# Performance work log

Hardware: AMD Instinct MI355X
Metric: run time of the kernel (lower is better)

Reference implementation:

```python
import jax, jax.numpy as jnp
import numpy as np

# Dimensions (match init_kwargs / input_specs)
B, S, D = 4, 2048, 1024
H, DK = 16, 64
CL = 64            # chunk_len
C, N, NL = 32, 2, 128  # chunks, neighbors, neighbor_len
EPS = 1e-5
SCALE = 1.0 / np.sqrt(DK)


def setup_inputs() -> dict:
    key = jax.random.key(0)
    ks = jax.random.split(key, 8)
    w_in = 1.0 / np.sqrt(D)   # xavier-like scale for projections
    return {
        "h": jax.random.normal(ks[0], (B, S, D), jnp.float32),
        "e": jax.random.normal(ks[1], (B, C, N, NL, D), jnp.float32),
        "ln_g": jnp.ones((D,), jnp.float32),
        "ln_b": jnp.zeros((D,), jnp.float32),
        "Wq": jax.random.normal(ks[2], (D, H * DK), jnp.float32) * w_in,
        "bq": jnp.zeros((H * DK,), jnp.float32),
        "Wk": jax.random.normal(ks[3], (D, H * DK), jnp.float32) * w_in,
        "bk": jnp.zeros((H * DK,), jnp.float32),
        "Wv": jax.random.normal(ks[4], (D, H * DK), jnp.float32) * w_in,
        "bv": jnp.zeros((H * DK,), jnp.float32),
        "Wo": jax.random.normal(ks[5], (H * DK, D), jnp.float32) * (1.0 / np.sqrt(H * DK)),
        "bo": jnp.zeros((D,), jnp.float32),
    }


def _layernorm(x, g, b):
    mu = jnp.mean(x, axis=-1, keepdims=True)
    var = jnp.mean(jnp.square(x - mu), axis=-1, keepdims=True)
    return (x - mu) * jax.lax.rsqrt(var + EPS) * g + b


def reference(h, e, ln_g, ln_b, Wq, bq, Wk, bk, Wv, bv, Wo, bo):
    residual = h
    # shift queries so each chunk attends to neighbors retrieved for the previous chunk
    hs = _layernorm(h[:, CL - 1:], ln_g, ln_b)          # [B, S-CL+1, D]
    total = C * CL
    pad = max(0, total - hs.shape[1])
    hp = jnp.pad(hs, ((0, 0), (0, pad), (0, 0))) if pad > 0 else hs[:, :total]
    hb = hp.reshape(B, C, CL, D)                         # [B,C,CL,D]

    q = (hb @ Wq + bq).reshape(B, C, CL, H, DK)
    k = (e @ Wk + bk).reshape(B, C, N, NL, H, DK)
    v = (e @ Wv + bv).reshape(B, C, N, NL, H, DK)

    # scores: [B, C, H, CL, N, NL], softmax over merged (N, NL)
    attn = jnp.einsum('bcihd,bcnjhd->bchinj', q, k) * SCALE
    sh = attn.shape
    attn = jax.nn.softmax(attn.reshape(sh[0], sh[1], sh[2], sh[3], -1), axis=-1).reshape(sh)

    o = jnp.einsum('bchinj,bcnjhd->bcihd', attn, v).reshape(B, C * CL, H * DK)
    o = o @ Wo + bo                                      # [B, C*CL, D]
    # shift output back and crop to original length
    o = jnp.pad(o, ((0, 0), (CL - 1, 0), (0, 0)))[:, :S]
    return o + residual
```

## Files before the change

kernel.cpp:

```cpp
#include <hip/hip_runtime.h>


typedef __attribute__((ext_vector_type(8))) short short8;
typedef __attribute__((ext_vector_type(4))) float f32x4;
typedef unsigned short ushort_t;
typedef unsigned long long u64;

__device__ inline ushort_t f2bf(float f) {
  union { float f; unsigned int u; } v; v.f = f;
  unsigned int u = v.u;
  return (ushort_t)((u + 0x7fffu + ((u >> 16) & 1u)) >> 16);
}
__device__ inline float bf2f(ushort_t s) {
  union { unsigned int u; float f; } v; v.u = ((unsigned int)s) << 16;
  return v.f;
}

__device__ inline void gl_lds16(const void* g, void* l) {
  __builtin_amdgcn_global_load_lds(
      (const __attribute__((address_space(1))) unsigned int*)g,
      (__attribute__((address_space(3))) unsigned int*)l, 16, 0, 0);
}

__global__ void transpose_w4(const float* __restrict__ W0, const float* __restrict__ W1,
                             const float* __restrict__ W2, const float* __restrict__ W3,
                             ushort_t* __restrict__ T0, ushort_t* __restrict__ T1,
                             ushort_t* __restrict__ T2, ushort_t* __restrict__ T3) {
  __shared__ float tile[32][33];
  const int z = blockIdx.z;
  const float* W = (z == 0) ? W0 : (z == 1) ? W1 : (z == 2) ? W2 : W3;
  ushort_t* WT   = (z == 0) ? T0 : (z == 1) ? T1 : (z == 2) ? T2 : T3;
  int k0 = blockIdx.x * 32, n0 = blockIdx.y * 32;
  int c = threadIdx.x & 31, r = threadIdx.x >> 5;
#pragma unroll
  for (int p = 0; p < 4; p++)
    tile[r + p * 8][c] = W[(size_t)(k0 + r + p * 8) * 1024 + n0 + c];
  __syncthreads();
#pragma unroll
  for (int p = 0; p < 4; p++)
    WT[(size_t)(n0 + r + p * 8) * 1024 + k0 + c] = f2bf(tile[c][r + p * 8]);
}

__global__ void ln_kernel(const float* __restrict__ h, const float* __restrict__ g,
                          const float* __restrict__ bb, ushort_t* __restrict__ hb) {
  int row = blockIdx.x;
  int b = row >> 11, jj = row & 2047;
  int t = threadIdx.x;
  ushort_t* dst = hb + (size_t)row * 1024;
  if (jj >= 1985) {
    ((unsigned int*)dst)[t] = 0u;
    ((unsigned int*)dst)[t + 256] = 0u;
    return;
  }
  const float* src = h + ((size_t)(b << 11) + jj + 63) * 1024;
  f32x4 x = *(const f32x4*)&src[t * 4];
  float s = x[0] + x[1] + x[2] + x[3];
  float sq = x[0]*x[0] + x[1]*x[1] + x[2]*x[2] + x[3]*x[3];
#pragma unroll
  for (int off = 32; off > 0; off >>= 1) {
    s  += __shfl_xor(s, off);
    sq += __shfl_xor(sq, off);
  }
  __shared__ float red[8];
  if ((t & 63) == 0) { red[(t >> 6) * 2] = s; red[(t >> 6) * 2 + 1] = sq; }
  __syncthreads();
  float sum = red[0] + red[2] + red[4] + red[6];
  float sumsq = red[1] + red[3] + red[5] + red[7];
  float mu = sum * (1.f / 1024.f);
  float var = sumsq * (1.f / 1024.f) - mu * mu;
  float rs = rsqrtf(var + 1e-5f);
  f32x4 gg = *(const f32x4*)&g[t * 4];
  f32x4 bv = *(const f32x4*)&bb[t * 4];
  ushort_t o0 = f2bf((x[0] - mu) * rs * gg[0] + bv[0]);
  ushort_t o1 = f2bf((x[1] - mu) * rs * gg[1] + bv[1]);
  ushort_t o2 = f2bf((x[2] - mu) * rs * gg[2] + bv[2]);
  ushort_t o3 = f2bf((x[3] - mu) * rs * gg[3] + bv[3]);
  u64 pack = (u64)o0 | ((u64)o1 << 16) | ((u64)o2 << 32) | ((u64)o3 << 48);
  *(u64*)&dst[t * 4] = pack;
}

__global__ void conv_bf16(const float* __restrict__ s, ushort_t* __restrict__ d, int n8) {
  int i = blockIdx.x * 256 + threadIdx.x;
  if (i >= n8) return;
  const f32x4* sp = (const f32x4*)(s + (size_t)i * 8);
  f32x4 a = sp[0], b = sp[1];
  short8 o;
  o[0] = (short)f2bf(a[0]); o[1] = (short)f2bf(a[1]);
  o[2] = (short)f2bf(a[2]); o[3] = (short)f2bf(a[3]);
  o[4] = (short)f2bf(b[0]); o[5] = (short)f2bf(b[1]);
  o[6] = (short)f2bf(b[2]); o[7] = (short)f2bf(b[3]);
  *(short8*)(d + (size_t)i * 8) = o;
}

template <int EPI>
__launch_bounds__(256, 2)
__global__ void gemm_bt(const ushort_t* __restrict__ A, const ushort_t* __restrict__ BT,
                        const float* __restrict__ bias, ushort_t* __restrict__ Cb,
                        float* __restrict__ Cf, const float* __restrict__ resid) {
  __shared__ __attribute__((aligned(16))) ushort_t lds[32768];
  const int bid = blockIdx.x, cpx = gridDim.x >> 3;
  const int swz = (bid & 7) * cpx + (bid >> 3);
  const int tm = (swz >> 3) * 128, tn = (swz & 7) * 128;
  const int t = threadIdx.x, lane = t & 63, wv = t >> 6;
  const int wm = (wv >> 1) * 64, wn = (wv & 1) * 64;
  const int row16 = lane & 15, g = lane >> 4;

  const int c0 = t, c1 = t + 256;
  const int ra0 = c0 >> 2, sa0 = ((c0 & 3) ^ ((ra0 >> 1) & 3)) * 8;
  const int ra1 = c1 >> 2, sa1 = ((c1 & 3) ^ ((ra1 >> 1) & 3)) * 8;
  const ushort_t* Ag0 = A + (size_t)(tm + ra0) * 1024 + sa0;
  const ushort_t* Ag1 = A + (size_t)(tm + ra1) * 1024 + sa1;
  const ushort_t* Bg0 = BT + (size_t)(tn + ra0) * 1024 + sa0;
  const ushort_t* Bg1 = BT + (size_t)(tn + ra1) * 1024 + sa1;

#define STG_A(T) { ushort_t* L_ = lds + ((T) & 3) * 8192; const int k0_ = (T) * 32; \
    gl_lds16(Ag0 + k0_, L_ + c0 * 8); gl_lds16(Ag1 + k0_, L_ + c1 * 8); }
#define STG_B(T) { ushort_t* L_ = lds + ((T) & 3) * 8192; const int k0_ = (T) * 32; \
    gl_lds16(Bg0 + k0_, L_ + 4096 + c0 * 8); gl_lds16(Bg1 + k0_, L_ + 4096 + c1 * 8); }

  int aoff[4], boff[4];
#pragma unroll
  for (int m = 0; m < 4; m++) {
    int ra = wm + m * 16 + row16;
    aoff[m] = ra * 32 + (g ^ ((ra >> 1) & 3)) * 8;
  }
#pragma unroll
  for (int n = 0; n < 4; n++) {
    int rb = wn + n * 16 + row16;
    boff[n] = 4096 + rb * 32 + (g ^ ((rb >> 1) & 3)) * 8;
  }

  f32x4 acc[4][4] = {};
  STG_A(0); STG_B(0); STG_A(1); STG_B(1);
  for (int T = 0; T < 32; ++T) {
    const ushort_t* Lb = lds + (T & 3) * 8192;
    if (T < 31) { asm volatile("s_waitcnt vmcnt(4)" ::: "memory"); }
    else        { asm volatile("s_waitcnt vmcnt(0)" ::: "memory"); }
    __builtin_amdgcn_s_barrier();
    short8 af0, af1;
    short8 bfv[4];
#pragma unroll
    for (int n = 0; n < 4; n++) bfv[n] = *(const short8*)&Lb[boff[n]];
    af0 = *(const short8*)&Lb[aoff[0]];
    af1 = *(const short8*)&Lb[aoff[1]];
    if (T < 30) STG_A(T + 2);
    __builtin_amdgcn_s_barrier();
    asm volatile("s_waitcnt lgkmcnt(0)" ::: "memory");
    __builtin_amdgcn_sched_barrier(0);
    __builtin_amdgcn_s_setprio(1);
#pragma unroll
    for (int n = 0; n < 4; n++) {
      acc[0][n] = __builtin_amdgcn_mfma_f32_16x16x32_bf16(af0, bfv[n], acc[0][n], 0, 0, 0);
      acc[1][n] = __builtin_amdgcn_mfma_f32_16x16x32_bf16(af1, bfv[n], acc[1][n], 0, 0, 0);
    }
    __builtin_amdgcn_s_setprio(0);
    __builtin_amdgcn_s_barrier();
    af0 = *(const short8*)&Lb[aoff[2]];
    af1 = *(const short8*)&Lb[aoff[3]];
    if (T < 30) STG_B(T + 2);
    __builtin_amdgcn_s_barrier();
    asm volatile("s_waitcnt lgkmcnt(0)" ::: "memory");
    __builtin_amdgcn_sched_barrier(0);
    __builtin_amdgcn_s_setprio(1);
#pragma unroll
    for (int n = 0; n < 4; n++) {
      acc[2][n] = __builtin_amdgcn_mfma_f32_16x16x32_bf16(af0, bfv[n], acc[2][n], 0, 0, 0);
      acc[3][n] = __builtin_amdgcn_mfma_f32_16x16x32_bf16(af1, bfv[n], acc[3][n], 0, 0, 0);
    }
    __builtin_amdgcn_s_setprio(0);
  }
#undef STG_A
#undef STG_B

  const int cr = g * 4, cc = row16;
  if (EPI == 0) {
    const int cb = tn + wn;
    float bsv[4];
#pragma unroll
    for (int n = 0; n < 4; n++) bsv[n] = bias[cb + n * 16 + cc];
#pragma unroll
    for (int m = 0; m < 4; m++) {
      int rbase = tm + wm + m * 16 + cr;
#pragma unroll
      for (int j = 0; j < 4; j++) {
        u64 pack = (u64)f2bf(acc[m][0][j] + bsv[0])
                 | ((u64)f2bf(acc[m][1][j] + bsv[1]) << 16)
                 | ((u64)f2bf(acc[m][2][j] + bsv[2]) << 32)
                 | ((u64)f2bf(acc[m][3][j] + bsv[3]) << 48);
        *(u64*)&Cb[(size_t)(rbase + j) * 1024 + cb + cc * 4] = pack;
      }
    }
  } else {
#pragma unroll
    for (int m = 0; m < 4; m++) {
#pragma unroll
      for (int n = 0; n < 4; n++) {
        int col = tn + wn + n * 16 + cc;
        float bsv = bias[col];
#pragma unroll
        for (int j = 0; j < 4; j++) {
          int rg = tm + wm + m * 16 + cr + j;
          float v = acc[m][n][j] + bsv;
          int b = rg >> 11, jj = rg & 2047;
          if (jj < 1985) {
            size_t oi = ((size_t)(b << 11) + jj + 63) * 1024 + col;
            Cf[oi] = v + resid[oi];
          }
        }
      }
    }
  }
}

__launch_bounds__(512, 2)
__global__ void kv_attn(const ushort_t* __restrict__ A, const ushort_t* __restrict__ WkvT,
                        const float* __restrict__ bk, const float* __restrict__ bv,
                        const ushort_t* __restrict__ Qb, ushort_t* __restrict__ Ob) {
  __shared__ __attribute__((aligned(16))) ushort_t smem[74752];
  ushort_t* lds = smem;
  const int bid = blockIdx.x;
  const int swz = (bid & 7) * 128 + (bid >> 3);
  const int bc = swz >> 3, hp = swz & 7;
  const int tm = bc * 256;
  const int t = threadIdx.x, lane = t & 63, wv = t >> 6;
  const int wm = wv >> 2, wn = wv & 3;
  const int row16 = lane & 15, g = lane >> 4;

  const int d1 = t + 512;
  const int ra0 = t >> 2, sa0 = ((t & 3) ^ ((ra0 >> 1) & 3)) * 8;
  const int ra1 = d1 >> 2, sa1 = ((d1 & 3) ^ ((ra1 >> 1) & 3)) * 8;
  const ushort_t* Ag0 = A + (size_t)(tm + ra0) * 1024 + sa0;
  const ushort_t* Ag1 = A + (size_t)(tm + ra1) * 1024 + sa1;
  const ushort_t* Bg0 = WkvT + (size_t)(hp * 128 + ra0) * 1024 + sa0;
  const ushort_t* Bg1 = WkvT + (size_t)(1024 + hp * 128 + (ra1 - 128)) * 1024 + sa1;

#define STG256_A(T) { ushort_t* L_ = lds + ((T) & 3) * 16384; const int k0_ = (T) * 32; \
    gl_lds16(Ag0 + k0_, L_ + t * 8); gl_lds16(Ag1 + k0_, L_ + d1 * 8); }
#define STG256_B(T) { ushort_t* L_ = lds + ((T) & 3) * 16384; const int k0_ = (T) * 32; \
    gl_lds16(Bg0 + k0_, L_ + 8192 + t * 8); gl_lds16(Bg1 + k0_, L_ + 8192 + d1 * 8); }

  int aoff[8], boff[4];
#pragma unroll
  for (int m = 0; m < 8; m++) {
    int ra = wm * 128 + m * 16 + row16;
    aoff[m] = ra * 32 + (g ^ ((ra >> 1) & 3)) * 8;
  }
#pragma unroll
  for (int n = 0; n < 4; n++) {
    int rb = wn * 64 + n * 16 + row16;
    boff[n] = 8192 + rb * 32 + (g ^ ((rb >> 1) & 3)) * 8;
  }

  f32x4 acc[8][4] = {};
  STG256_A(0); STG256_B(0); STG256_A(1); STG256_B(1);
  for (int T = 0; T < 32; ++T) {
    const ushort_t* Lb = lds + (T & 3) * 16384;
    if (T < 31) { asm volatile("s_waitcnt vmcnt(4)" ::: "memory"); }
    else        { asm volatile("s_waitcnt vmcnt(0)" ::: "memory"); }
    __builtin_amdgcn_s_barrier();
    short8 af[4], bfv[4];
#pragma unroll
    for (int n = 0; n < 4; n++) bfv[n] = *(const short8*)&Lb[boff[n]];
#pragma unroll
    for (int m = 0; m < 4; m++) af[m] = *(const short8*)&Lb[aoff[m]];
    if (T < 30) STG256_A(T + 2);
    __builtin_amdgcn_s_barrier();
    asm volatile("s_waitcnt lgkmcnt(0)" ::: "memory");
    __builtin_amdgcn_sched_barrier(0);
    __builtin_amdgcn_s_setprio(1);
#pragma unroll
    for (int m = 0; m < 4; m++)
#pragma unroll
      for (int n = 0; n < 4; n++)
        acc[m][n] = __builtin_amdgcn_mfma_f32_16x16x32_bf16(af[m], bfv[n], acc[m][n], 0, 0, 0);
    __builtin_amdgcn_s_setprio(0);
    __builtin_amdgcn_s_barrier();
#pragma unroll
    for (int m = 0; m < 4; m++) af[m] = *(const short8*)&Lb[aoff[4 + m]];
    if (T < 30) STG256_B(T + 2);
    __builtin_amdgcn_s_barrier();
    asm volatile("s_waitcnt lgkmcnt(0)" ::: "memory");
    __builtin_amdgcn_sched_barrier(0);
    __builtin_amdgcn_s_setprio(1);
#pragma unroll
    for (int m = 0; m < 4; m++)
#pragma unroll
      for (int n = 0; n < 4; n++)
        acc[4 + m][n] = __builtin_amdgcn_mfma_f32_16x16x32_bf16(af[m], bfv[n], acc[4 + m][n], 0, 0, 0);
    __builtin_amdgcn_s_setprio(0);
  }
#undef STG256_A
#undef STG256_B

  __syncthreads();

  if (wn < 2) {
    ushort_t* KsH = smem + (wn ? 24576 : 4096);
    float bsv[4];
#pragma unroll
    for (int n = 0; n < 4; n++) bsv[n] = bk[hp * 128 + wn * 64 + n * 16 + row16];
    const int slot = ((row16 >> 1) << 3) + (row16 & 1) * 4;
#pragma unroll
    for (int m = 0; m < 8; m++) {
      int krow0 = wm * 128 + m * 16 + g * 4;
#pragma unroll
      for (int j = 0; j < 4; j++) {
        int krow = krow0 + j;
        u64 pack = (u64)f2bf(acc[m][0][j] + bsv[0])
                 | ((u64)f2bf(acc[m][1][j] + bsv[1]) << 16)
                 | ((u64)f2bf(acc[m][2][j] + bsv[2]) << 32)
                 | ((u64)f2bf(acc[m][3][j] + bsv[3]) << 48);
        int sl = ((row16 >> 1) ^ (krow & 7)) * 8 + (row16 & 1) * 4;
        *(u64*)&KsH[krow * 64 + sl] = pack;
      }
    }
    (void)slot;
  } else {
    ushort_t* VtH = smem + 40960 + (wn & 1) * 16896;
    float bsv[4];
#pragma unroll
    for (int n = 0; n < 4; n++) bsv[n] = bv[hp * 128 + (wn - 2) * 64 + n * 16 + row16];
#pragma unroll
    for (int m = 0; m < 8; m++) {
      int krow0 = wm * 128 + m * 16 + g * 4;
#pragma unroll
      for (int n = 0; n < 4; n++) {
        int od = n * 16 + row16;
        u64 pack = (u64)f2bf(acc[m][n][0] + bsv[n])
                 | ((u64)f2bf(acc[m][n][1] + bsv[n]) << 16)
                 | ((u64)f2bf(acc[m][n][2] + bsv[n]) << 32)
                 | ((u64)f2bf(acc[m][n][3] + bsv[n]) << 48);
        *(u64*)&VtH[od * 264 + krow0] = pack;
      }
    }
  }
  {
    const int hb2 = t >> 8, tl = t & 255;
    ushort_t* QsH = smem + (hb2 ? 20480 : 0);
    size_t qbase = ((size_t)bc * 64) * 1024 + (hp * 2 + hb2) * 64;
    int ch = tl, r = ch >> 3, gq = (ch & 7) ^ (r & 7);
    gl_lds16(Qb + qbase + (size_t)r * 1024 + gq * 8, &QsH[ch * 8]);
    ch = tl + 256; r = ch >> 3; gq = (ch & 7) ^ (r & 7);
    gl_lds16(Qb + qbase + (size_t)r * 1024 + gq * 8, &QsH[ch * 8]);
  }
  __syncthreads();

  const int tl = t & 255, hb2 = t >> 8;
  const int wvL = tl >> 6, laneL = tl & 63;
  ushort_t* QsH = smem + (hb2 ? 20480 : 0);
  ushort_t* KsH = QsH + 4096;
  ushort_t* SpH = QsH;
  ushort_t* VtH = smem + 40960 + hb2 * 16896;

  const int rowA = laneL & 15, kgA = (laneL >> 4) * 8;
  const int cswz = (rowA & 7) << 3;
  f32x4 accs[4][4] = {};
#pragma unroll
  for (int kk = 0; kk < 64; kk += 32) {
    int cq = ((kk + kgA) ^ cswz);
    short8 af[4], bfr[4];
#pragma unroll
    for (int m = 0; m < 4; m++) af[m] = *(const short8*)&QsH[(m * 16 + rowA) * 64 + cq];
#pragma unroll
    for (int n = 0; n < 4; n++)
      bfr[n] = *(const short8*)&KsH[(wvL * 64 + n * 16 + rowA) * 64 + cq];
#pragma unroll
    for (int m = 0; m < 4; m++)
#pragma unroll
      for (int n = 0; n < 4; n++)
        accs[m][n] = __builtin_amdgcn_mfma_f32_16x16x32_bf16(af[m], bfr[n], accs[m][n], 0, 0, 0);
  }
  __syncthreads();

  {
    const int cr = (laneL >> 4) * 4, cc = laneL & 15;
#pragma unroll
    for (int m = 0; m < 4; m++)
#pragma unroll
      for (int n = 0; n < 4; n++)
#pragma unroll
        for (int j = 0; j < 4; j++)
          SpH[(m * 16 + cr + j) * 264 + wvL * 64 + n * 16 + cc] = f2bf(accs[m][n][j]);
  }
  __syncthreads();

  {
    const int r = tl >> 2, q = tl & 3;
    const int base = r * 264 + q * 64;
    float ev[64];
#pragma unroll
    for (int p = 0; p < 8; p++) {
      short8 sv = *(const short8*)&SpH[base + p * 8];
#pragma unroll
      for (int i = 0; i < 8; i++) ev[p * 8 + i] = bf2f((ushort_t)sv[i]);
    }
    float mx = ev[0];
#pragma unroll
    for (int i = 1; i < 64; i++) mx = fmaxf(mx, ev[i]);
    mx = fmaxf(mx, __shfl_xor(mx, 1));
    mx = fmaxf(mx, __shfl_xor(mx, 2));
    float sum = 0.f;
#pragma unroll
    for (int i = 0; i < 64; i++) {
      ev[i] = __expf((ev[i] - mx) * 0.125f);
      sum += ev[i];
    }
    sum += __shfl_xor(sum, 1);
    sum += __shfl_xor(sum, 2);
    float inv = 1.f / sum;
#pragma unroll
    for (int p = 0; p < 8; p++) {
      short8 pv;
#pragma unroll
      for (int i = 0; i < 8; i++) pv[i] = (short)f2bf(ev[p * 8 + i] * inv);
      *(short8*)&SpH[base + p * 8] = pv;
    }
  }
  __syncthreads();

  {
    f32x4 acco[4] = {};
#pragma unroll
    for (int kt = 0; kt < 8; kt++) {
      short8 bfv = *(const short8*)&VtH[(wvL * 16 + rowA) * 264 + kt * 32 + kgA];
#pragma unroll
      for (int m = 0; m < 4; m++) {
        short8 af = *(const short8*)&SpH[(m * 16 + rowA) * 264 + kt * 32 + kgA];
        acco[m] = __builtin_amdgcn_mfma_f32_16x16x32_bf16(af, bfv, acco[m], 0, 0, 0);
      }
    }
    const int cr = (laneL >> 4) * 4, cc = laneL & 15;
    size_t obase = ((size_t)bc * 64) * 1024 + (hp * 2 + hb2) * 64 + wvL * 16 + cc;
#pragma unroll
    for (int m = 0; m < 4; m++)
#pragma unroll
      for (int j = 0; j < 4; j++)
        Ob[obase + (size_t)(m * 16 + cr + j) * 1024] = f2bf(acco[m][j]);
  }
}

__global__ void copy_prologue(const float* __restrict__ h, float* __restrict__ out) {
  int tt = blockIdx.x;
  int b = tt / 63, r = tt % 63;
  size_t idx = ((size_t)(b * 2048) + r) * 1024 + threadIdx.x * 4;
  *(f32x4*)&out[idx] = *(const f32x4*)&h[idx];
}

extern "C" void kernel_launch(void* const* d_in, const int* in_sizes, int n_in,
                              void* d_out, int out_size, void* d_ws, size_t ws_size,
                              hipStream_t stream) {
  const float* h    = (const float*)d_in[0];
  const float* e    = (const float*)d_in[1];
  const float* ln_g = (const float*)d_in[2];
  const float* ln_b = (const float*)d_in[3];
  const float* Wq   = (const float*)d_in[4];
  const float* bq   = (const float*)d_in[5];
  const float* Wk   = (const float*)d_in[6];
  const float* bk   = (const float*)d_in[7];
  const float* Wv   = (const float*)d_in[8];
  const float* bv   = (const float*)d_in[9];
  const float* Wo   = (const float*)d_in[10];
  const float* bo   = (const float*)d_in[11];
  float* out = (float*)d_out;

  char* ws = (char*)d_ws;
  const size_t MB = 1024 * 1024;
  ushort_t* WqT  = (ushort_t*)(ws + 0 * MB);
  ushort_t* WkT  = (ushort_t*)(ws + 2 * MB);
  ushort_t* WvT  = (ushort_t*)(ws + 4 * MB);
  ushort_t* WoT  = (ushort_t*)(ws + 6 * MB);
  ushort_t* hb   = (ushort_t*)(ws + 8 * MB);
  ushort_t* e_bf = (ushort_t*)(ws + 24 * MB);
  ushort_t* Qb   = (ushort_t*)(ws + 88 * MB);
  ushort_t* Obuf = (ushort_t*)(ws + 104 * MB);

  transpose_w4<<<dim3(32, 32, 4), 256, 0, stream>>>(Wq, Wk, Wv, Wo, WqT, WkT, WvT, WoT);

  ln_kernel<<<8192, 256, 0, stream>>>(h, ln_g, ln_b, hb);
  conv_bf16<<<16384, 256, 0, stream>>>(e, e_bf, 4194304);

  gemm_bt<0><<<512, 256, 0, stream>>>(hb, WqT, bq, Qb, nullptr, nullptr);
  kv_attn<<<1024, 512, 0, stream>>>(e_bf, WkT, bk, bv, Qb, Obuf);

  gemm_bt<1><<<512, 256, 0, stream>>>(Obuf, WoT, bo, nullptr, out, h);
  copy_prologue<<<252, 256, 0, stream>>>(h, out);
}
```

Before: 269.3 us.

## Merge prep kernels, fold prologue copy into output GEMM, prefetch Q early

Fuses the weight transpose, layernorm and e-to-bf16 conversion into a single launch with block-range dispatch, and folds the residual prologue copy into the output GEMM as extra blocks. In the attention kernel, the Q tile load is moved to a dedicated LDS region and issued at kernel start so it overlaps the KV projection, with the K/V/score buffers relaid out to make room. The aim is fewer kernel launches and less tail idle time, at the cost of slightly more shared memory and a hardcoded swizzle constant in the GEMM.

Measured after the change: 258.4 us. -4.0%, faster.

```diff
diff --git a/kernel.cpp b/kernel.cpp
--- a/kernel.cpp
+++ b/kernel.cpp
@@ -22,74 +22,78 @@
       (__attribute__((address_space(3))) unsigned int*)l, 16, 0, 0);
 }
 
-__global__ void transpose_w4(const float* __restrict__ W0, const float* __restrict__ W1,
-                             const float* __restrict__ W2, const float* __restrict__ W3,
-                             ushort_t* __restrict__ T0, ushort_t* __restrict__ T1,
-                             ushort_t* __restrict__ T2, ushort_t* __restrict__ T3) {
+__global__ void prep_kernel(const float* __restrict__ W0, const float* __restrict__ W1,
+                            const float* __restrict__ W2, const float* __restrict__ W3,
+                            ushort_t* __restrict__ T0, ushort_t* __restrict__ T1,
+                            ushort_t* __restrict__ T2, ushort_t* __restrict__ T3,
+                            const float* __restrict__ h, const float* __restrict__ lg,
+                            const float* __restrict__ lb, ushort_t* __restrict__ hb,
+                            const float* __restrict__ e, ushort_t* __restrict__ e_bf) {
   __shared__ float tile[32][33];
-  const int z = blockIdx.z;
-  const float* W = (z == 0) ? W0 : (z == 1) ? W1 : (z == 2) ? W2 : W3;
-  ushort_t* WT   = (z == 0) ? T0 : (z == 1) ? T1 : (z == 2) ? T2 : T3;
-  int k0 = blockIdx.x * 32, n0 = blockIdx.y * 32;
-  int c = threadIdx.x & 31, r = threadIdx.x >> 5;
-#pragma unroll
-  for (int p = 0; p < 4; p++)
-    tile[r + p * 8][c] = W[(size_t)(k0 + r + p * 8) * 1024 + n0 + c];
-  __syncthreads();
-#pragma unroll
-  for (int p = 0; p < 4; p++)
-    WT[(size_t)(n0 + r + p * 8) * 1024 + k0 + c] = f2bf(tile[c][r + p * 8]);
-}
-
-__global__ void ln_kernel(const float* __restrict__ h, const float* __restrict__ g,
-                          const float* __restrict__ bb, ushort_t* __restrict__ hb) {
-  int row = blockIdx.x;
-  int b = row >> 11, jj = row & 2047;
-  int t = threadIdx.x;
-  ushort_t* dst = hb + (size_t)row * 1024;
-  if (jj >= 1985) {
-    ((unsigned int*)dst)[t] = 0u;
-    ((unsigned int*)dst)[t + 256] = 0u;
+  __shared__ float red[8];
+  const int blk = blockIdx.x, t = threadIdx.x;
+
+  if (blk < 4096) {
+    const int z = blk >> 10, xy = blk & 1023;
+    const float* W = (z == 0) ? W0 : (z == 1) ? W1 : (z == 2) ? W2 : W3;
+    ushort_t* WT   = (z == 0) ? T0 : (z == 1) ? T1 : (z == 2) ? T2 : T3;
+    int k0 = (xy & 31) * 32, n0 = (xy >> 5) * 32;
+    int c = t & 31, r = t >> 5;
+#pragma unroll
+    for (int p = 0; p < 4; p++)
+      tile[r + p * 8][c] = W[(size_t)(k0 + r + p * 8) * 1024 + n0 + c];
+    __syncthreads();
+#pragma unroll
+    for (int p = 0; p < 4; p++)
+      WT[(size_t)(n0 + r + p * 8) * 1024 + k0 + c] = f2bf(tile[c][r + p * 8]);
     return;
   }
-  const float* src = h + ((size_t)(b << 11) + jj + 63) * 1024;
-  f32x4 x = *(const f32x4*)&src[t * 4];
-  float s = x[0] + x[1] + x[2] + x[3];
-  float sq = x[0]*x[0] + x[1]*x[1] + x[2]*x[2] + x[3]*x[3];
-#pragma unroll
-  for (int off = 32; off > 0; off >>= 1) {
-    s  += __shfl_xor(s, off);
-    sq += __shfl_xor(sq, off);
-  }
-  __shared__ float red[8];
-  if ((t & 63) == 0) { red[(t >> 6) * 2] = s; red[(t >> 6) * 2 + 1] = sq; }
-  __syncthreads();
-  float sum = red[0] + red[2] + red[4] + red[6];
-  float sumsq = red[1] + red[3] + red[5] + red[7];
-  float mu = sum * (1.f / 1024.f);
-  float var = sumsq * (1.f / 1024.f) - mu * mu;
-  float rs = rsqrtf(var + 1e-5f);
-  f32x4 gg = *(const f32x4*)&g[t * 4];
-  f32x4 bv = *(const f32x4*)&bb[t * 4];
-  ushort_t o0 = f2bf((x[0] - mu) * rs * gg[0] + bv[0]);
-  ushort_t o1 = f2bf((x[1] - mu) * rs * gg[1] + bv[1]);
-  ushort_t o2 = f2bf((x[2] - mu) * rs * gg[2] + bv[2]);
-  ushort_t o3 = f2bf((x[3] - mu) * rs * gg[3] + bv[3]);
-  u64 pack = (u64)o0 | ((u64)o1 << 16) | ((u64)o2 << 32) | ((u64)o3 << 48);
-  *(u64*)&dst[t * 4] = pack;
-}
-
-__global__ void conv_bf16(const float* __restrict__ s, ushort_t* __restrict__ d, int n8) {
-  int i = blockIdx.x * 256 + threadIdx.x;
-  if (i >= n8) return;
-  const f32x4* sp = (const f32x4*)(s + (size_t)i * 8);
-  f32x4 a = sp[0], b = sp[1];
-  short8 o;
-  o[0] = (short)f2bf(a[0]); o[1] = (short)f2bf(a[1]);
-  o[2] = (short)f2bf(a[2]); o[3] = (short)f2bf(a[3]);
-  o[4] = (short)f2bf(b[0]); o[5] = (short)f2bf(b[1]);
-  o[6] = (short)f2bf(b[2]); o[7] = (short)f2bf(b[3]);
-  *(short8*)(d + (size_t)i * 8) = o;
+  if (blk < 12288) {
+    int row = blk - 4096;
+    int b = row >> 11, jj = row & 2047;
+    ushort_t* dst = hb + (size_t)row * 1024;
+    if (jj >= 1985) {
+      ((unsigned int*)dst)[t] = 0u;
+      ((unsigned int*)dst)[t + 256] = 0u;
+      return;
+    }
+    const float* src = h + ((size_t)(b << 11) + jj + 63) * 1024;
+    f32x4 x = *(const f32x4*)&src[t * 4];
+    float s = x[0] + x[1] + x[2] + x[3];
+    float sq = x[0]*x[0] + x[1]*x[1] + x[2]*x[2] + x[3]*x[3];
+#pragma unroll
+    for (int off = 32; off > 0; off >>= 1) {
+      s  += __shfl_xor(s, off);
+      sq += __shfl_xor(sq, off);
+    }
+    if ((t & 63) == 0) { red[(t >> 6) * 2] = s; red[(t >> 6) * 2 + 1] = sq; }
+    __syncthreads();
+    float sum = red[0] + red[2] + red[4] + red[6];
+    float sumsq = red[1] + red[3] + red[5] + red[7];
+    float mu = sum * (1.f / 1024.f);
+    float var = sumsq * (1.f / 1024.f) - mu * mu;
+    float rs = rsqrtf(var + 1e-5f);
+    f32x4 gg = *(const f32x4*)&lg[t * 4];
+    f32x4 bv = *(const f32x4*)&lb[t * 4];
+    ushort_t o0 = f2bf((x[0] - mu) * rs * gg[0] + bv[0]);
+    ushort_t o1 = f2bf((x[1] - mu) * rs * gg[1] + bv[1]);
+    ushort_t o2 = f2bf((x[2] - mu) * rs * gg[2] + bv[2]);
+    ushort_t o3 = f2bf((x[3] - mu) * rs * gg[3] + bv[3]);
+    u64 pack = (u64)o0 | ((u64)o1 << 16) | ((u64)o2 << 32) | ((u64)o3 << 48);
+    *(u64*)&dst[t * 4] = pack;
+    return;
+  }
+  {
+    int i = (blk - 12288) * 256 + t;
+    const f32x4* sp = (const f32x4*)(e + (size_t)i * 8);
+    f32x4 a = sp[0], b = sp[1];
+    short8 o;
+    o[0] = (short)f2bf(a[0]); o[1] = (short)f2bf(a[1]);
+    o[2] = (short)f2bf(a[2]); o[3] = (short)f2bf(a[3]);
+    o[4] = (short)f2bf(b[0]); o[5] = (short)f2bf(b[1]);
+    o[6] = (short)f2bf(b[2]); o[7] = (short)f2bf(b[3]);
+    *(short8*)(e_bf + (size_t)i * 8) = o;
+  }
 }
 
 template <int EPI>
@@ -97,8 +101,16 @@
 __global__ void gemm_bt(const ushort_t* __restrict__ A, const ushort_t* __restrict__ BT,
                         const float* __restrict__ bias, ushort_t* __restrict__ Cb,
                         float* __restrict__ Cf, const float* __restrict__ resid) {
+  const int bid = blockIdx.x;
+  if (EPI == 1 && bid >= 512) {
+    int tt = bid - 512;
+    int b = tt / 63, r = tt % 63;
+    size_t idx = ((size_t)(b * 2048) + r) * 1024 + threadIdx.x * 4;
+    *(f32x4*)&Cf[idx] = *(const f32x4*)&resid[idx];
+    return;
+  }
   __shared__ __attribute__((aligned(16))) ushort_t lds[32768];
-  const int bid = blockIdx.x, cpx = gridDim.x >> 3;
+  const int cpx = 64;
   const int swz = (bid & 7) * cpx + (bid >> 3);
   const int tm = (swz >> 3) * 128, tn = (swz & 7) * 128;
   const int t = threadIdx.x, lane = t & 63, wv = t >> 6;
@@ -216,7 +228,7 @@
 __global__ void kv_attn(const ushort_t* __restrict__ A, const ushort_t* __restrict__ WkvT,
                         const float* __restrict__ bk, const float* __restrict__ bv,
                         const ushort_t* __restrict__ Qb, ushort_t* __restrict__ Ob) {
-  __shared__ __attribute__((aligned(16))) ushort_t smem[74752];
+  __shared__ __attribute__((aligned(16))) ushort_t smem[75776];
   ushort_t* lds = smem;
   const int bid = blockIdx.x;
   const int swz = (bid & 7) * 128 + (bid >> 3);
@@ -226,6 +238,16 @@
   const int wm = wv >> 2, wn = wv & 3;
   const int row16 = lane & 15, g = lane >> 4;
 
+  {
+    const int hb2q = t >> 8, tlq = t & 255;
+    ushort_t* QsH = smem + 67584 + hb2q * 4096;
+    size_t qbase = ((size_t)bc * 64) * 1024 + (hp * 2 + hb2q) * 64;
+    int ch = tlq, r = ch >> 3, gq = (ch & 7) ^ (r & 7);
+    gl_lds16(Qb + qbase + (size_t)r * 1024 + gq * 8, &QsH[ch * 8]);
+    ch = tlq + 256; r = ch >> 3; gq = (ch & 7) ^ (r & 7);
+    gl_lds16(Qb + qbase + (size_t)r * 1024 + gq * 8, &QsH[ch * 8]);
+  }
+
   const int d1 = t + 512;
   const int ra0 = t >> 2, sa0 = ((t & 3) ^ ((ra0 >> 1) & 3)) * 8;
   const int ra1 = d1 >> 2, sa1 = ((d1 & 3) ^ ((ra1 >> 1) & 3)) * 8;
@@ -295,11 +317,10 @@
   __syncthreads();
 
   if (wn < 2) {
-    ushort_t* KsH = smem + (wn ? 24576 : 4096);
+    ushort_t* KsH = smem + wn * 16896;
     float bsv[4];
 #pragma unroll
     for (int n = 0; n < 4; n++) bsv[n] = bk[hp * 128 + wn * 64 + n * 16 + row16];
-    const int slot = ((row16 >> 1) << 3) + (row16 & 1) * 4;
 #pragma unroll
     for (int m = 0; m < 8; m++) {
       int krow0 = wm * 128 + m * 16 + g * 4;
@@ -314,9 +335,8 @@
         *(u64*)&KsH[krow * 64 + sl] = pack;
       }
     }
-    (void)slot;
   } else {
-    ushort_t* VtH = smem + 40960 + (wn & 1) * 16896;
+    ushort_t* VtH = smem + 33792 + (wn & 1) * 16896;
     float bsv[4];
 #pragma unroll
     for (int n = 0; n < 4; n++) bsv[n] = bv[hp * 128 + (wn - 2) * 64 + n * 16 + row16];
@@ -334,23 +354,14 @@
       }
     }
   }
-  {
-    const int hb2 = t >> 8, tl = t & 255;
-    ushort_t* QsH = smem + (hb2 ? 20480 : 0);
-    size_t qbase = ((size_t)bc * 64) * 1024 + (hp * 2 + hb2) * 64;
-    int ch = tl, r = ch >> 3, gq = (ch & 7) ^ (r & 7);
-    gl_lds16(Qb + qbase + (size_t)r * 1024 + gq * 8, &QsH[ch * 8]);
-    ch = tl + 256; r = ch >> 3; gq = (ch & 7) ^ (r & 7);
-    gl_lds16(Qb + qbase + (size_t)r * 1024 + gq * 8, &QsH[ch * 8]);
-  }
   __syncthreads();
 
   const int tl = t & 255, hb2 = t >> 8;
   const int wvL = tl >> 6, laneL = tl & 63;
-  ushort_t* QsH = smem + (hb2 ? 20480 : 0);
-  ushort_t* KsH = QsH + 4096;
-  ushort_t* SpH = QsH;
-  ushort_t* VtH = smem + 40960 + hb2 * 16896;
+  ushort_t* QsH = smem + 67584 + hb2 * 4096;
+  ushort_t* KsH = smem + hb2 * 16896;
+  ushort_t* SpH = KsH;
+  ushort_t* VtH = smem + 33792 + hb2 * 16896;
 
   const int rowA = laneL & 15, kgA = (laneL >> 4) * 8;
   const int cswz = (rowA & 7) << 3;
@@ -437,13 +448,6 @@
       for (int j = 0; j < 4; j++)
         Ob[obase + (size_t)(m * 16 + cr + j) * 1024] = f2bf(acco[m][j]);
   }
-}
-
-__global__ void copy_prologue(const float* __restrict__ h, float* __restrict__ out) {
-  int tt = blockIdx.x;
-  int b = tt / 63, r = tt % 63;
-  size_t idx = ((size_t)(b * 2048) + r) * 1024 + threadIdx.x * 4;
-  *(f32x4*)&out[idx] = *(const f32x4*)&h[idx];
 }
 
 extern "C" void kernel_launch(void* const* d_in, const int* in_sizes, int n_in,
@@ -474,14 +478,11 @@
   ushort_t* Qb   = (ushort_t*)(ws + 88 * MB);
   ushort_t* Obuf = (ushort_t*)(ws + 104 * MB);
 
-  transpose_w4<<<dim3(32, 32, 4), 256, 0, stream>>>(Wq, Wk, Wv, Wo, WqT, WkT, WvT, WoT);
-
-  ln_kernel<<<8192, 256, 0, stream>>>(h, ln_g, ln_b, hb);
-  conv_bf16<<<16384, 256, 0, stream>>>(e, e_bf, 4194304);
+  prep_kernel<<<28672, 256, 0, stream>>>(Wq, Wk, Wv, Wo, WqT, WkT, WvT, WoT,
+                                         h, ln_g, ln_b, hb, e, e_bf);
 
   gemm_bt<0><<<512, 256, 0, stream>>>(hb, WqT, bq, Qb, nullptr, nullptr);
   kv_attn<<<1024, 512, 0, stream>>>(e_bf, WkT, bk, bv, Qb, Obuf);
 
-  gemm_bt<1><<<512, 256, 0, stream>>>(Obuf, WoT, bo, nullptr, out, h);
-  copy_prologue<<<252, 256, 0, stream>>>(h, out);
-}
+  gemm_bt<1><<<764, 256, 0, stream>>>(Obuf, WoT, bo, nullptr, out, h);
+}
```
